# Optimization experiments

Measured on AMD Instinct MI355X. Metric: run time of the kernel, lower is better.

The kernel has to match this reference:

```python
import jax, jax.numpy as jnp
import numpy as np
import math

N = 4096
D = 256


def _xavier(key, shape):
    fan_in, fan_out = shape[0], shape[1]
    std = math.sqrt(2.0 / (fan_in + fan_out))
    return jax.random.normal(key, shape, dtype=jnp.float32) * std


def setup_inputs() -> dict:
    key = jax.random.key(0)
    ks = jax.random.split(key, 12)
    return {
        "cur": jax.random.normal(ks[0], (N, D), dtype=jnp.float32),
        "pre": jax.random.normal(ks[1], (N, D), dtype=jnp.float32),
        # SpatialHyperedge params
        "r_proj_s": _xavier(ks[2], (D, D)),
        "incidence_s": _xavier(ks[3], (N, N - 1)),
        # TemporalHyperedge params
        "r_proj_t": _xavier(ks[4], (D, D)),
        "incidence_t": _xavier(ks[5], (N, N)),
        # HHNodeMP params
        "node_proj": _xavier(ks[6], (D, D)),
        "spa_edge_proj": _xavier(ks[7], (D, D)),
        "tmp_edge_proj": _xavier(ks[8], (D, D)),
        "theta_w": _xavier(ks[9], (D, D)),
        "theta_b": jnp.zeros((D,), dtype=jnp.float32),
    }


def _scatter_slave(vals):
    """Place [N, N-1] per-row slave values into a zero-diagonal [N, N] matrix.
    Row i's k-th slave is column k if k < i else k+1 (all j != i in order)."""
    n = vals.shape[0]
    k = jnp.arange(n - 1)[None, :]
    cols = k + (k >= jnp.arange(n)[:, None])  # [N, N-1] column indices
    rows = jnp.broadcast_to(jnp.arange(n)[:, None], (n, n - 1))
    return jnp.zeros((n, n), dtype=vals.dtype).at[rows.reshape(-1), cols.reshape(-1)].set(vals.reshape(-1))


def _fro(x):
    return jnp.sqrt(jnp.sum(x * x))


def reference(cur, pre, r_proj_s, incidence_s, r_proj_t, incidence_t,
              node_proj, spa_edge_proj, tmp_edge_proj, theta_w, theta_b):
    n, d = cur.shape
    inv_sqrt_d = 1.0 / math.sqrt(d)

    # ---- SpatialHyperedge ----
    Xd = jax.lax.stop_gradient(cur)
    master_s = Xd @ r_proj_s                                   # [N, D]
    M_s_full = _scatter_slave(incidence_s)                     # [N, N], zero diag
    neigh_recon_s = M_s_full @ Xd                              # == bmm over gathered slaves
    spatial_loss = (_fro(master_s - neigh_recon_s) * 0.2
                    + jnp.sum(jnp.abs(incidence_s))
                    + 0.001 * _fro(incidence_s))
    # clamp(min=0) then zero-out entries not strictly > 0  => relu-like
    clipped_s = jnp.where(incidence_s > 0.0, incidence_s, 0.0)
    incidence_all = _scatter_slave(clipped_s) + jnp.eye(n, dtype=cur.dtype)

    # ---- TemporalHyperedge ----
    cur_d = jax.lax.stop_gradient(cur)
    pre_d = jax.lax.stop_gradient(pre)
    master_t = cur_d @ r_proj_t
    neigh_recon_t = incidence_t @ pre_d
    temporal_loss = (_fro(master_t - neigh_recon_t) * 0.2
                     + jnp.sum(jnp.abs(incidence_t))
                     + 0.001 * _fro(incidence_t))
    incidence_t_clipped = jnp.maximum(incidence_t, 0.0)

    # ---- SpatialHyperedgeMP ----
    spa_edge_fea = incidence_all @ cur
    spa_deg = jnp.sum(incidence_all, axis=1, keepdims=True)
    spa_emb = spa_edge_fea / spa_deg                           # [N, D]

    # ---- TemporalHyperedgeMP ----
    tmp_edge_fea = incidence_t_clipped @ pre + cur
    tmp_deg = jnp.sum(incidence_t_clipped, axis=1, keepdims=True) + 1.0
    tmp_emb = tmp_edge_fea / tmp_deg                           # [N, D]

    # ---- HHNodeMP ----
    node_fea = cur @ node_proj
    spa_fea = spa_emb @ spa_edge_proj
    tmp_fea = tmp_emb @ tmp_edge_proj
    spa_attn = jnp.sum(spa_fea * node_fea, axis=1, keepdims=True) * inv_sqrt_d
    tmp_attn = jnp.sum(tmp_fea * node_fea, axis=1, keepdims=True) * inv_sqrt_d
    val = spa_attn * spa_fea + tmp_attn * tmp_fea
    node_emb = jax.nn.relu(val @ theta_w.T + theta_b)          # dropout = identity (eval)

    return node_emb, temporal_loss + spatial_loss
```

## Files before the change

kernel.cpp:

```cpp
#include <hip/hip_runtime.h>
#include <hip/hip_bf16.h>
#include <math.h>

#define NN 4096
#define DD 256

typedef __bf16 bf16x8 __attribute__((ext_vector_type(8)));
typedef short  short8 __attribute__((ext_vector_type(8)));
typedef float  f32x4  __attribute__((ext_vector_type(4)));

#define MFMA16(a, b, c) __builtin_amdgcn_mfma_f32_16x16x32_bf16((a), (b), (c), 0, 0, 0)

__device__ inline bf16x8 brelu(bf16x8 a) {
    short8 s = __builtin_bit_cast(short8, a);
    s = s & ~(s >> 15);
    return __builtin_bit_cast(bf16x8, s);
}

__device__ inline float wave_red(float v) {
#pragma unroll
    for (int o = 32; o > 0; o >>= 1) v += __shfl_down(v, o, 64);
    return v;
}

__device__ inline unsigned short bfbits(float f) {
    return __builtin_bit_cast(unsigned short, (__bf16)f);
}

__global__ __launch_bounds__(256) void k_prep(const float* __restrict__ cur,
                                              const float* __restrict__ pre,
                                              __bf16* __restrict__ cur_bf,
                                              __bf16* __restrict__ curT,
                                              __bf16* __restrict__ preT) {
    const int z = blockIdx.z;
    const int i0 = blockIdx.x * 64, d0 = blockIdx.y * 64;
    const float* src = z ? pre : cur;
    __bf16* dstT = z ? preT : curT;
    __shared__ unsigned short tile[64][72];
    const int t = threadIdx.x;
    const int r = t >> 2, c4 = (t & 3) * 16;
    const float* srow = src + (size_t)(i0 + r) * DD + d0 + c4;
    alignas(16) unsigned short loc[16];
#pragma unroll
    for (int e = 0; e < 4; ++e) {
        float4 v = ((const float4*)srow)[e];
        loc[e * 4 + 0] = bfbits(v.x);
        loc[e * 4 + 1] = bfbits(v.y);
        loc[e * 4 + 2] = bfbits(v.z);
        loc[e * 4 + 3] = bfbits(v.w);
    }
#pragma unroll
    for (int e = 0; e < 16; ++e) tile[r][c4 + e] = loc[e];
    if (z == 0) {
        __bf16* drow = cur_bf + (size_t)(i0 + r) * DD + d0 + c4;
        *(uint4*)drow = *(uint4*)&loc[0];
        *(uint4*)(drow + 8) = *(uint4*)&loc[8];
    }
    __syncthreads();
    alignas(16) unsigned short o[16];
#pragma unroll
    for (int e = 0; e < 16; ++e) o[e] = tile[c4 + e][r];
    __bf16* trow = dstT + (size_t)(d0 + r) * NN + i0 + c4;
    *(uint4*)trow = *(uint4*)&o[0];
    *(uint4*)(trow + 8) = *(uint4*)&o[8];
}

__global__ __launch_bounds__(256) void k_proj(
    const float* __restrict__ a0, const float* __restrict__ a1, const float* __restrict__ a2,
    const float* __restrict__ a3, const float* __restrict__ a4, const float* __restrict__ a5,
    __bf16* __restrict__ o0, __bf16* __restrict__ o1, __bf16* __restrict__ o2,
    __bf16* __restrict__ o3, __bf16* __restrict__ o4, __bf16* __restrict__ o5) {
    const int id = blockIdx.y, r = blockIdx.x, t = threadIdx.x;
    const float* src = id == 0 ? a0 : id == 1 ? a1 : id == 2 ? a2 : id == 3 ? a3 : id == 4 ? a4 : a5;
    __bf16* dst = id == 0 ? o0 : id == 1 ? o1 : id == 2 ? o2 : id == 3 ? o3 : id == 4 ? o4 : o5;
    float v = src[r * DD + t];
    if (id < 5) dst[t * DD + r] = (__bf16)v;
    else        dst[r * DD + t] = (__bf16)v;
}

__global__ __launch_bounds__(256) void k_conv_t(const float* __restrict__ inc,
                                                __bf16* __restrict__ Mbf,
                                                float* __restrict__ rowsum,
                                                float* __restrict__ pAbs, float* __restrict__ pSq) {
    const int i = blockIdx.x, t = threadIdx.x;
    const float4* src = (const float4*)(inc + (size_t)i * NN);
    ushort4* dst = (ushort4*)(Mbf + (size_t)i * NN);
    float rs = 0.f, as = 0.f, qs = 0.f;
#pragma unroll
    for (int e = 0; e < 4; ++e) {
        const int f = t + 256 * e;
        float4 v = src[f];
        float x[4] = {v.x, v.y, v.z, v.w};
        unsigned short o[4];
#pragma unroll
        for (int j = 0; j < 4; ++j) {
            float fv = x[j];
            as += fabsf(fv); qs += fv * fv; rs += fmaxf(fv, 0.f);
            o[j] = bfbits(fv);
        }
        dst[f] = make_ushort4(o[0], o[1], o[2], o[3]);
    }
    __shared__ float red[3][4];
    const int w = t >> 6, lane = t & 63;
    rs = wave_red(rs); as = wave_red(as); qs = wave_red(qs);
    if (lane == 0) { red[0][w] = rs; red[1][w] = as; red[2][w] = qs; }
    __syncthreads();
    if (t == 0) {
        rowsum[i] = red[0][0] + red[0][1] + red[0][2] + red[0][3];
        pAbs[i]   = red[1][0] + red[1][1] + red[1][2] + red[1][3];
        pSq[i]    = red[2][0] + red[2][1] + red[2][2] + red[2][3];
    }
}

__global__ __launch_bounds__(256) void k_conv_s(const float* __restrict__ inc,
                                                __bf16* __restrict__ Mbf,
                                                float* __restrict__ rowsum,
                                                float* __restrict__ pAbs, float* __restrict__ pSq) {
    const int i = blockIdx.x, t = threadIdx.x;
    __shared__ unsigned short row[NN];
    const float* srow = inc + (size_t)i * (NN - 1);
    float rs = 0.f, as = 0.f, qs = 0.f;
#pragma unroll
    for (int e = 0; e < 4; ++e) {
        const int f = t + 256 * e;
        float x[4] = {0.f, 0.f, 0.f, 0.f};
        if (f < 1023) __builtin_memcpy(x, srow + 4 * f, 16);
        else          __builtin_memcpy(x, srow + 4092, 12);
#pragma unroll
        for (int j = 0; j < 4; ++j) {
            const int k = 4 * f + j;
            float fv = x[j];
            as += fabsf(fv); qs += fv * fv; rs += fmaxf(fv, 0.f);
            if (k < NN - 1) row[k + (k >= i)] = bfbits(fv);
        }
    }
    if (t == 0) row[i] = 0;
    __syncthreads();
    uint4* dOut = (uint4*)(Mbf + (size_t)i * NN);
    const uint4* sIn = (const uint4*)row;
    dOut[t] = sIn[t];
    dOut[t + 256] = sIn[t + 256];
    __shared__ float red[3][4];
    const int w = t >> 6, lane = t & 63;
    rs = wave_red(rs); as = wave_red(as); qs = wave_red(qs);
    if (lane == 0) { red[0][w] = rs; red[1][w] = as; red[2][w] = qs; }
    __syncthreads();
    if (t == 0) {
        rowsum[i] = red[0][0] + red[0][1] + red[0][2] + red[0][3];
        pAbs[i]   = red[1][0] + red[1][1] + red[1][2] + red[1][3];
        pSq[i]    = red[2][0] + red[2][1] + red[2][2] + red[2][3];
    }
}

template <int DUAL>
__device__ inline void mfma_step(const __bf16 (&As)[64][72], const __bf16 (&Bs)[64][72],
                                 int wr, int wc, int quad, int l16,
                                 f32x4 (&accR)[2][2], f32x4 (&accL)[2][2]) {
#pragma unroll
    for (int ks = 0; ks < 2; ++ks) {
        const int kc = ks * 32 + quad * 8;
        bf16x8 a0 = *(const bf16x8*)&As[wr * 32 + l16][kc];
        bf16x8 a1 = *(const bf16x8*)&As[wr * 32 + 16 + l16][kc];
        bf16x8 b0 = *(const bf16x8*)&Bs[wc * 32 + l16][kc];
        bf16x8 b1 = *(const bf16x8*)&Bs[wc * 32 + 16 + l16][kc];
        accR[0][0] = MFMA16(a0, b0, accR[0][0]);
        accR[0][1] = MFMA16(a0, b1, accR[0][1]);
        accR[1][0] = MFMA16(a1, b0, accR[1][0]);
        accR[1][1] = MFMA16(a1, b1, accR[1][1]);
        if (DUAL) {
            bf16x8 a0r = brelu(a0), a1r = brelu(a1);
            accL[0][0] = MFMA16(a0r, b0, accL[0][0]);
            accL[0][1] = MFMA16(a0r, b1, accL[0][1]);
            accL[1][0] = MFMA16(a1r, b0, accL[1][0]);
            accL[1][1] = MFMA16(a1r, b1, accL[1][1]);
        }
    }
}

__global__ __launch_bounds__(256) void k_big(const __bf16* __restrict__ Mt, const __bf16* __restrict__ Ms,
                                             const __bf16* __restrict__ preT, const __bf16* __restrict__ curT,
                                             const float* __restrict__ negMt, const float* __restrict__ negMs,
                                             const float* __restrict__ cur,
                                             float* __restrict__ feaT, float* __restrict__ feaS,
                                             float* __restrict__ pDiff) {
    const int z = blockIdx.z;
    const __bf16* A  = z ? Ms : Mt;
    const __bf16* BT = z ? curT : preT;
    const float* negM = z ? negMs : negMt;
    float* fea = z ? feaS : feaT;
    const int n0 = blockIdx.x * 64, m0 = blockIdx.y * 64;
    __shared__ __bf16 As[64][72], Bs[64][72];
    __shared__ float sred[4];
    f32x4 accR[2][2], accL[2][2];
#pragma unroll
    for (int i = 0; i < 2; ++i)
#pragma unroll
        for (int j = 0; j < 2; ++j) { accR[i][j] = (f32x4)0.f; accL[i][j] = (f32x4)0.f; }
    const int t = threadIdx.x, w = t >> 6, lane = t & 63, quad = lane >> 4, l16 = lane & 15;
    const int wr = w >> 1, wc = w & 1;
    const int sr = t >> 2, sc = (t & 3) * 16;
    const __bf16* gA = A + (size_t)(m0 + sr) * NN + sc;
    const __bf16* gB = BT + (size_t)(n0 + sr) * NN + sc;
    for (int kt = 0; kt < NN / 64; ++kt) {
        uint4 av0 = *(const uint4*)(gA);
        uint4 av1 = *(const uint4*)(gA + 8);
        uint4 bv0 = *(const uint4*)(gB);
        uint4 bv1 = *(const uint4*)(gB + 8);
        __syncthreads();
        *(uint4*)&As[sr][sc] = av0; *(uint4*)&As[sr][sc + 8] = av1;
        *(uint4*)&Bs[sr][sc] = bv0; *(uint4*)&Bs[sr][sc + 8] = bv1;
        __syncthreads();
        mfma_step<1>(As, Bs, wr, wc, quad, l16, accR, accL);
        gA += 64; gB += 64;
    }
    float sumd = 0.f;
#pragma unroll
    for (int mi = 0; mi < 2; ++mi)
#pragma unroll
        for (int ni = 0; ni < 2; ++ni)
#pragma unroll
            for (int r = 0; r < 4; ++r) {
                int gr = m0 + wr * 32 + mi * 16 + quad * 4 + r;
                int gc = n0 + wc * 32 + ni * 16 + l16;
                size_t idx = (size_t)gr * DD + gc;
                float diff = accR[mi][ni][r] + negM[idx];
                sumd += diff * diff;
                fea[idx] = accL[mi][ni][r] + cur[idx];
            }
    sumd = wave_red(sumd);
    if (lane == 0) sred[w] = sumd;
    __syncthreads();
    if (t == 0)
        pDiff[z * 256 + blockIdx.y * 4 + blockIdx.x] = sred[0] + sred[1] + sred[2] + sred[3];
}

__global__ __launch_bounds__(256) void k_small3(const __bf16* __restrict__ cur_bf,
                                                const __bf16* __restrict__ pTs, const __bf16* __restrict__ pTt,
                                                const __bf16* __restrict__ pTn,
                                                float* __restrict__ negMs, float* __restrict__ negMt,
                                                float* __restrict__ nodeFea) {
    const int z = blockIdx.z;
    const __bf16* BT = z == 0 ? pTs : (z == 1 ? pTt : pTn);
    const int n0 = blockIdx.x * 64, m0 = blockIdx.y * 64;
    __shared__ __bf16 As[64][72], Bs[64][72];
    f32x4 accR[2][2];
#pragma unroll
    for (int i = 0; i < 2; ++i)
#pragma unroll
        for (int j = 0; j < 2; ++j) accR[i][j] = (f32x4)0.f;
    const int t = threadIdx.x, w = t >> 6, lane = t & 63, quad = lane >> 4, l16 = lane & 15;
    const int wr = w >> 1, wc = w & 1;
    const int sr = t >> 2, sc = (t & 3) * 16;
    const __bf16* gA = cur_bf + (size_t)(m0 + sr) * DD + sc;
    const __bf16* gB = BT + (size_t)(n0 + sr) * DD + sc;
    for (int kt = 0; kt < DD / 64; ++kt) {
        uint4 av0 = *(const uint4*)(gA);
        uint4 av1 = *(const uint4*)(gA + 8);
        uint4 bv0 = *(const uint4*)(gB);
        uint4 bv1 = *(const uint4*)(gB + 8);
        __syncthreads();
        *(uint4*)&As[sr][sc] = av0; *(uint4*)&As[sr][sc + 8] = av1;
        *(uint4*)&Bs[sr][sc] = bv0; *(uint4*)&Bs[sr][sc + 8] = bv1;
        __syncthreads();
        mfma_step<0>(As, Bs, wr, wc, quad, l16, accR, accR);
        gA += 64; gB += 64;
    }
#pragma unroll
    for (int mi = 0; mi < 2; ++mi)
#pragma unroll
        for (int ni = 0; ni < 2; ++ni)
#pragma unroll
            for (int r = 0; r < 4; ++r) {
                int gr = m0 + wr * 32 + mi * 16 + quad * 4 + r;
                int gc = n0 + wc * 32 + ni * 16 + l16;
                size_t idx = (size_t)gr * DD + gc;
                float v = accR[mi][ni][r];
                if (z == 0) negMs[idx] = -v;
                else if (z == 1) negMt[idx] = -v;
                else nodeFea[idx] = v;
            }
}

__global__ __launch_bounds__(256) void k_fea(const float* __restrict__ feaS, const float* __restrict__ feaT,
                                             const float* __restrict__ rsS, const float* __restrict__ rsT,
                                             const __bf16* __restrict__ pTspa, const __bf16* __restrict__ pTtmp,
                                             float* __restrict__ spaF, float* __restrict__ tmpF) {
    const int z = blockIdx.z;
    const float* fea = z ? feaT : feaS;
    const float* rs = z ? rsT : rsS;
    const __bf16* BT = z ? pTtmp : pTspa;
    float* outF = z ? tmpF : spaF;
    const int n0 = blockIdx.x * 64, m0 = blockIdx.y * 64;
    __shared__ __bf16 As[64][72], Bs[64][72];
    f32x4 accR[2][2];
#pragma unroll
    for (int i = 0; i < 2; ++i)
#pragma unroll
        for (int j = 0; j < 2; ++j) accR[i][j] = (f32x4)0.f;
    const int t = threadIdx.x, w = t >> 6, lane = t & 63, quad = lane >> 4, l16 = lane & 15;
    const int wr = w >> 1, wc = w & 1;
    const int sr = t >> 2, sc = (t & 3) * 16;
    const float inv = 1.f / (rs[m0 + sr] + 1.f);
    const float* gA = fea + (size_t)(m0 + sr) * DD + sc;
    const __bf16* gB = BT + (size_t)(n0 + sr) * DD + sc;
    for (int kt = 0; kt < DD / 64; ++kt) {
        __bf16 tmp[16];
#pragma unroll
        for (int e4 = 0; e4 < 4; ++e4) {
            float4 v = ((const float4*)gA)[e4];
            tmp[e4 * 4 + 0] = (__bf16)(v.x * inv);
            tmp[e4 * 4 + 1] = (__bf16)(v.y * inv);
            tmp[e4 * 4 + 2] = (__bf16)(v.z * inv);
            tmp[e4 * 4 + 3] = (__bf16)(v.w * inv);
        }
        uint4 bv0 = *(const uint4*)(gB);
        uint4 bv1 = *(const uint4*)(gB + 8);
        __syncthreads();
        *(uint4*)&As[sr][sc] = *(uint4*)&tmp[0]; *(uint4*)&As[sr][sc + 8] = *(uint4*)&tmp[8];
        *(uint4*)&Bs[sr][sc] = bv0; *(uint4*)&Bs[sr][sc + 8] = bv1;
        __syncthreads();
        mfma_step<0>(As, Bs, wr, wc, quad, l16, accR, accR);
        gA += 64; gB += 64;
    }
#pragma unroll
    for (int mi = 0; mi < 2; ++mi)
#pragma unroll
        for (int ni = 0; ni < 2; ++ni)
#pragma unroll
            for (int r = 0; r < 4; ++r) {
                int gr = m0 + wr * 32 + mi * 16 + quad * 4 + r;
                int gc = n0 + wc * 32 + ni * 16 + l16;
                outF[(size_t)gr * DD + gc] = accR[mi][ni][r];
            }
}

__global__ __launch_bounds__(256) void k_attn(const float* __restrict__ spaF, const float* __restrict__ tmpF,
                                              const float* __restrict__ nodeF,
                                              float* __restrict__ spaA, float* __restrict__ tmpA) {
    const int t = threadIdx.x, w = t >> 6, lane = t & 63;
    const int i = blockIdx.x * 4 + w;
    const float4* sf = (const float4*)(spaF + (size_t)i * DD);
    const float4* tf = (const float4*)(tmpF + (size_t)i * DD);
    const float4* nf = (const float4*)(nodeF + (size_t)i * DD);
    float4 s = sf[lane], p = tf[lane], n = nf[lane];
    float ds = s.x * n.x + s.y * n.y + s.z * n.z + s.w * n.w;
    float dt = p.x * n.x + p.y * n.y + p.z * n.z + p.w * n.w;
    ds = wave_red(ds); dt = wave_red(dt);
    if (lane == 0) { spaA[i] = ds * 0.0625f; tmpA[i] = dt * 0.0625f; }
}

__global__ __launch_bounds__(256) void k_final(const float* __restrict__ spaF, const float* __restrict__ tmpF,
                                               const float* __restrict__ spaA, const float* __restrict__ tmpA,
                                               const __bf16* __restrict__ thetaBf, const float* __restrict__ thetaB,
                                               float* __restrict__ out) {
    const int n0 = blockIdx.x * 64, m0 = blockIdx.y * 64;
    __shared__ __bf16 As[64][72], Bs[64][72];
    f32x4 accR[2][2];
#pragma unroll
    for (int i = 0; i < 2; ++i)
#pragma unroll
        for (int j = 0; j < 2; ++j) accR[i][j] = (f32x4)0.f;
    const int t = threadIdx.x, w = t >> 6, lane = t & 63, quad = lane >> 4, l16 = lane & 15;
    const int wr = w >> 1, wc = w & 1;
    const int sr = t >> 2, sc = (t & 3) * 16;
    const float sa = spaA[m0 + sr], ta = tmpA[m0 + sr];
    const float* gS = spaF + (size_t)(m0 + sr) * DD + sc;
    const float* gT = tmpF + (size_t)(m0 + sr) * DD + sc;
    const __bf16* gB = thetaBf + (size_t)(n0 + sr) * DD + sc;
    for (int kt = 0; kt < DD / 64; ++kt) {
        __bf16 tmp[16];
#pragma unroll
        for (int e4 = 0; e4 < 4; ++e4) {
            float4 vs = ((const float4*)gS)[e4];
            float4 vt = ((const float4*)gT)[e4];
            tmp[e4 * 4 + 0] = (__bf16)(sa * vs.x + ta * vt.x);
            tmp[e4 * 4 + 1] = (__bf16)(sa * vs.y + ta * vt.y);
            tmp[e4 * 4 + 2] = (__bf16)(sa * vs.z + ta * vt.z);
            tmp[e4 * 4 + 3] = (__bf16)(sa * vs.w + ta * vt.w);
        }
        uint4 bv0 = *(const uint4*)(gB);
        uint4 bv1 = *(const uint4*)(gB + 8);
        __syncthreads();
        *(uint4*)&As[sr][sc] = *(uint4*)&tmp[0]; *(uint4*)&As[sr][sc + 8] = *(uint4*)&tmp[8];
        *(uint4*)&Bs[sr][sc] = bv0; *(uint4*)&Bs[sr][sc + 8] = bv1;
        __syncthreads();
        mfma_step<0>(As, Bs, wr, wc, quad, l16, accR, accR);
        gS += 64; gT += 64; gB += 64;
    }
#pragma unroll
    for (int mi = 0; mi < 2; ++mi)
#pragma unroll
        for (int ni = 0; ni < 2; ++ni)
#pragma unroll
            for (int r = 0; r < 4; ++r) {
                int gr = m0 + wr * 32 + mi * 16 + quad * 4 + r;
                int gc = n0 + wc * 32 + ni * 16 + l16;
                float v = accR[mi][ni][r] + thetaB[gc];
                out[(size_t)gr * DD + gc] = fmaxf(v, 0.f);
            }
}

__global__ __launch_bounds__(256) void k_loss(const float* __restrict__ pAbsT, const float* __restrict__ pSqT,
                                              const float* __restrict__ pAbsS, const float* __restrict__ pSqS,
                                              const float* __restrict__ pDiff,
                                              float* __restrict__ out) {
    const int t = threadIdx.x;
    float aT = 0.f, qT = 0.f, aS = 0.f, qS = 0.f;
#pragma unroll
    for (int j = 0; j < 16; ++j) {
        const int i = t + 256 * j;
        aT += pAbsT[i]; qT += pSqT[i]; aS += pAbsS[i]; qS += pSqS[i];
    }
    float dT = pDiff[t], dS = pDiff[256 + t];
    aT = wave_red(aT); qT = wave_red(qT); aS = wave_red(aS); qS = wave_red(qS);
    dT = wave_red(dT); dS = wave_red(dS);
    __shared__ float red[6][4];
    const int w = t >> 6, lane = t & 63;
    if (lane == 0) { red[0][w] = aT; red[1][w] = qT; red[2][w] = aS; red[3][w] = qS; red[4][w] = dT; red[5][w] = dS; }
    __syncthreads();
    if (t == 0) {
        float s[6];
#pragma unroll
        for (int k = 0; k < 6; ++k) s[k] = red[k][0] + red[k][1] + red[k][2] + red[k][3];
        float l = s[0] + 0.001f * sqrtf(s[1]) + 0.2f * sqrtf(s[4])
                + s[2] + 0.001f * sqrtf(s[3]) + 0.2f * sqrtf(s[5]);
        out[(size_t)NN * DD] = l;
    }
}

extern "C" void kernel_launch(void* const* d_in, const int* in_sizes, int n_in,
                              void* d_out, int out_size, void* d_ws, size_t ws_size,
                              hipStream_t stream) {
    (void)in_sizes; (void)n_in; (void)out_size; (void)ws_size;
    const float* cur      = (const float*)d_in[0];
    const float* pre      = (const float*)d_in[1];
    const float* r_proj_s = (const float*)d_in[2];
    const float* inc_s    = (const float*)d_in[3];
    const float* r_proj_t = (const float*)d_in[4];
    const float* inc_t    = (const float*)d_in[5];
    const float* node_pj  = (const float*)d_in[6];
    const float* spa_pj   = (const float*)d_in[7];
    const float* tmp_pj   = (const float*)d_in[8];
    const float* theta_w  = (const float*)d_in[9];
    const float* theta_b  = (const float*)d_in[10];
    float* out = (float*)d_out;

    char* p = (char*)d_ws;
    auto alloc = [&](size_t bytes) -> void* {
        void* r = (void*)p;
        p += (bytes + 255) & ~(size_t)255;
        return r;
    };
    __bf16* Mt      = (__bf16*)alloc((size_t)NN * NN * 2);
    __bf16* Ms      = (__bf16*)alloc((size_t)NN * NN * 2);
    __bf16* cur_bf  = (__bf16*)alloc((size_t)NN * DD * 2);
    __bf16* curT    = (__bf16*)alloc((size_t)NN * DD * 2);
    __bf16* preT    = (__bf16*)alloc((size_t)NN * DD * 2);
    __bf16* pTs     = (__bf16*)alloc((size_t)DD * DD * 2);
    __bf16* pTt     = (__bf16*)alloc((size_t)DD * DD * 2);
    __bf16* pTn     = (__bf16*)alloc((size_t)DD * DD * 2);
    __bf16* pTspa   = (__bf16*)alloc((size_t)DD * DD * 2);
    __bf16* pTtmp   = (__bf16*)alloc((size_t)DD * DD * 2);
    __bf16* thetaBf = (__bf16*)alloc((size_t)DD * DD * 2);
    float* negMs    = (float*)alloc((size_t)NN * DD * 4);
    float* negMt    = (float*)alloc((size_t)NN * DD * 4);
    float* nodeFea  = (float*)alloc((size_t)NN * DD * 4);
    float* feaS     = (float*)alloc((size_t)NN * DD * 4);
    float* feaT     = (float*)alloc((size_t)NN * DD * 4);
    float* spaF     = (float*)alloc((size_t)NN * DD * 4);
    float* tmpF     = (float*)alloc((size_t)NN * DD * 4);
    float* rsS      = (float*)alloc((size_t)NN * 4);
    float* rsT      = (float*)alloc((size_t)NN * 4);
    float* spaA     = (float*)alloc((size_t)NN * 4);
    float* tmpA     = (float*)alloc((size_t)NN * 4);
    float* pAbsT    = (float*)alloc((size_t)NN * 4);
    float* pSqT     = (float*)alloc((size_t)NN * 4);
    float* pAbsS    = (float*)alloc((size_t)NN * 4);
    float* pSqS     = (float*)alloc((size_t)NN * 4);
    float* pDiff    = (float*)alloc(512 * 4);

    k_prep<<<dim3(NN / 64, DD / 64, 2), 256, 0, stream>>>(cur, pre, cur_bf, curT, preT);
    k_proj<<<dim3(DD, 6), 256, 0, stream>>>(r_proj_s, r_proj_t, node_pj, spa_pj, tmp_pj, theta_w,
                                            pTs, pTt, pTn, pTspa, pTtmp, thetaBf);
    k_conv_t<<<NN, 256, 0, stream>>>(inc_t, Mt, rsT, pAbsT, pSqT);
    k_conv_s<<<NN, 256, 0, stream>>>(inc_s, Ms, rsS, pAbsS, pSqS);
    k_small3<<<dim3(4, 64, 3), 256, 0, stream>>>(cur_bf, pTs, pTt, pTn, negMs, negMt, nodeFea);
    k_big<<<dim3(4, 64, 2), 256, 0, stream>>>(Mt, Ms, preT, curT, negMt, negMs, cur, feaT, feaS, pDiff);
    k_fea<<<dim3(4, 64, 2), 256, 0, stream>>>(feaS, feaT, rsS, rsT, pTspa, pTtmp, spaF, tmpF);
    k_attn<<<NN / 4, 256, 0, stream>>>(spaF, tmpF, nodeFea, spaA, tmpA);
    k_final<<<dim3(4, 64), 256, 0, stream>>>(spaF, tmpF, spaA, tmpA, thetaBf, theta_b, out);
    k_loss<<<1, 256, 0, stream>>>(pAbsT, pSqT, pAbsS, pSqS, pDiff, out);
}
```

Measured before the change: 268.8 us.

## Retile big GEMM to full-width 32-row tiles with double-buffered swizzled LDS; merge conv kernels

Measured after the change: 292.5 us. 8.8% more time.

```diff
diff --git a/kernel.cpp b/kernel.cpp
--- a/kernel.cpp
+++ b/kernel.cpp
@@ -78,78 +78,170 @@
     else        dst[r * DD + t] = (__bf16)v;
 }
 
-__global__ __launch_bounds__(256) void k_conv_t(const float* __restrict__ inc,
-                                                __bf16* __restrict__ Mbf,
-                                                float* __restrict__ rowsum,
-                                                float* __restrict__ pAbs, float* __restrict__ pSq) {
-    const int i = blockIdx.x, t = threadIdx.x;
-    const float4* src = (const float4*)(inc + (size_t)i * NN);
-    ushort4* dst = (ushort4*)(Mbf + (size_t)i * NN);
-    float rs = 0.f, as = 0.f, qs = 0.f;
-#pragma unroll
-    for (int e = 0; e < 4; ++e) {
-        const int f = t + 256 * e;
-        float4 v = src[f];
-        float x[4] = {v.x, v.y, v.z, v.w};
-        unsigned short o[4];
-#pragma unroll
-        for (int j = 0; j < 4; ++j) {
-            float fv = x[j];
-            as += fabsf(fv); qs += fv * fv; rs += fmaxf(fv, 0.f);
-            o[j] = bfbits(fv);
-        }
-        dst[f] = make_ushort4(o[0], o[1], o[2], o[3]);
-    }
-    __shared__ float red[3][4];
-    const int w = t >> 6, lane = t & 63;
-    rs = wave_red(rs); as = wave_red(as); qs = wave_red(qs);
-    if (lane == 0) { red[0][w] = rs; red[1][w] = as; red[2][w] = qs; }
-    __syncthreads();
-    if (t == 0) {
-        rowsum[i] = red[0][0] + red[0][1] + red[0][2] + red[0][3];
-        pAbs[i]   = red[1][0] + red[1][1] + red[1][2] + red[1][3];
-        pSq[i]    = red[2][0] + red[2][1] + red[2][2] + red[2][3];
-    }
-}
-
-__global__ __launch_bounds__(256) void k_conv_s(const float* __restrict__ inc,
-                                                __bf16* __restrict__ Mbf,
-                                                float* __restrict__ rowsum,
-                                                float* __restrict__ pAbs, float* __restrict__ pSq) {
+__global__ __launch_bounds__(256) void k_conv(const float* __restrict__ incT, const float* __restrict__ incS,
+                                              __bf16* __restrict__ Mt, __bf16* __restrict__ Ms,
+                                              float* __restrict__ rsT, float* __restrict__ rsS,
+                                              float* __restrict__ pAbsT, float* __restrict__ pSqT,
+                                              float* __restrict__ pAbsS, float* __restrict__ pSqS) {
     const int i = blockIdx.x, t = threadIdx.x;
     __shared__ unsigned short row[NN];
-    const float* srow = inc + (size_t)i * (NN - 1);
+    __shared__ float red[3][4];
     float rs = 0.f, as = 0.f, qs = 0.f;
-#pragma unroll
-    for (int e = 0; e < 4; ++e) {
-        const int f = t + 256 * e;
-        float x[4] = {0.f, 0.f, 0.f, 0.f};
-        if (f < 1023) __builtin_memcpy(x, srow + 4 * f, 16);
-        else          __builtin_memcpy(x, srow + 4092, 12);
-#pragma unroll
-        for (int j = 0; j < 4; ++j) {
-            const int k = 4 * f + j;
-            float fv = x[j];
-            as += fabsf(fv); qs += fv * fv; rs += fmaxf(fv, 0.f);
-            if (k < NN - 1) row[k + (k >= i)] = bfbits(fv);
-        }
-    }
-    if (t == 0) row[i] = 0;
+    if (blockIdx.y == 0) {
+        const float4* src = (const float4*)(incT + (size_t)i * NN);
+        ushort4* dst = (ushort4*)(Mt + (size_t)i * NN);
+#pragma unroll
+        for (int e = 0; e < 4; ++e) {
+            const int f = t + 256 * e;
+            float4 v = src[f];
+            float x[4] = {v.x, v.y, v.z, v.w};
+            unsigned short o[4];
+#pragma unroll
+            for (int j = 0; j < 4; ++j) {
+                float fv = x[j];
+                as += fabsf(fv); qs += fv * fv; rs += fmaxf(fv, 0.f);
+                o[j] = bfbits(fv);
+            }
+            dst[f] = make_ushort4(o[0], o[1], o[2], o[3]);
+        }
+        const int w = t >> 6, lane = t & 63;
+        rs = wave_red(rs); as = wave_red(as); qs = wave_red(qs);
+        if (lane == 0) { red[0][w] = rs; red[1][w] = as; red[2][w] = qs; }
+        __syncthreads();
+        if (t == 0) {
+            rsT[i]   = red[0][0] + red[0][1] + red[0][2] + red[0][3];
+            pAbsT[i] = red[1][0] + red[1][1] + red[1][2] + red[1][3];
+            pSqT[i]  = red[2][0] + red[2][1] + red[2][2] + red[2][3];
+        }
+    } else {
+        const float* srow = incS + (size_t)i * (NN - 1);
+#pragma unroll
+        for (int e = 0; e < 4; ++e) {
+            const int f = t + 256 * e;
+            float x[4] = {0.f, 0.f, 0.f, 0.f};
+            if (f < 1023) __builtin_memcpy(x, srow + 4 * f, 16);
+            else          __builtin_memcpy(x, srow + 4092, 12);
+#pragma unroll
+            for (int j = 0; j < 4; ++j) {
+                const int k = 4 * f + j;
+                float fv = x[j];
+                as += fabsf(fv); qs += fv * fv; rs += fmaxf(fv, 0.f);
+                if (k < NN - 1) row[k + (k >= i)] = bfbits(fv);
+            }
+        }
+        if (t == 0) row[i] = 0;
+        __syncthreads();
+        uint4* dOut = (uint4*)(Ms + (size_t)i * NN);
+        const uint4* sIn = (const uint4*)row;
+        dOut[t] = sIn[t];
+        dOut[t + 256] = sIn[t + 256];
+        const int w = t >> 6, lane = t & 63;
+        rs = wave_red(rs); as = wave_red(as); qs = wave_red(qs);
+        if (lane == 0) { red[0][w] = rs; red[1][w] = as; red[2][w] = qs; }
+        __syncthreads();
+        if (t == 0) {
+            rsS[i]   = red[0][0] + red[0][1] + red[0][2] + red[0][3];
+            pAbsS[i] = red[1][0] + red[1][1] + red[1][2] + red[1][3];
+            pSqS[i]  = red[2][0] + red[2][1] + red[2][2] + red[2][3];
+        }
+    }
+}
+
+__global__ __launch_bounds__(256) void k_big(const __bf16* __restrict__ Mt, const __bf16* __restrict__ Ms,
+                                             const __bf16* __restrict__ preT, const __bf16* __restrict__ curT,
+                                             const float* __restrict__ negMt, const float* __restrict__ negMs,
+                                             const float* __restrict__ cur,
+                                             float* __restrict__ feaT, float* __restrict__ feaS,
+                                             float* __restrict__ pDiff) {
+    const int z = blockIdx.y;
+    const __bf16* A  = z ? Ms : Mt;
+    const __bf16* BT = z ? curT : preT;
+    const float* negM = z ? negMs : negMt;
+    float* fea = z ? feaS : feaT;
+    const int m0 = blockIdx.x * 32;
+    __shared__ __bf16 As[2][32][64];
+    __shared__ float sred[4];
+    const int t = threadIdx.x, w = t >> 6, lane = t & 63, quad = lane >> 4, l16 = lane & 15;
+    const int rsw = l16 & 7;
+    const int srow = t >> 3, sc8 = t & 7;
+    const int swz = (sc8 ^ (srow & 7)) * 8;
+    const __bf16* gA = A + (size_t)(m0 + srow) * NN + sc8 * 8;
+    const int nb = w * 64;
+    const __bf16* gB[4];
+#pragma unroll
+    for (int nf = 0; nf < 4; ++nf)
+        gB[nf] = BT + (size_t)(nb + nf * 16 + l16) * NN + quad * 8;
+
+    f32x4 accR[2][4], accL[2][4];
+#pragma unroll
+    for (int mi = 0; mi < 2; ++mi)
+#pragma unroll
+        for (int nf = 0; nf < 4; ++nf) { accR[mi][nf] = (f32x4)0.f; accL[mi][nf] = (f32x4)0.f; }
+
+    bf16x8 b[2][2][4];
+    uint4 preA;
+    {
+        uint4 a0 = *(const uint4*)gA; gA += 64;
+        *(uint4*)&As[0][srow][swz] = a0;
+        preA = *(const uint4*)gA; gA += 64;
+#pragma unroll
+        for (int ks = 0; ks < 2; ++ks)
+#pragma unroll
+            for (int nf = 0; nf < 4; ++nf)
+                b[0][ks][nf] = *(const bf16x8*)(gB[nf] + ks * 32);
+        __syncthreads();
+    }
+#pragma unroll 2
+    for (int kt = 0; kt < 64; ++kt) {
+        const int cb = kt & 1;
+        if (kt < 63) *(uint4*)&As[cb ^ 1][srow][swz] = preA;
+        if (kt < 62) { preA = *(const uint4*)gA; gA += 64; }
+        if (kt < 63) {
+#pragma unroll
+            for (int ks = 0; ks < 2; ++ks)
+#pragma unroll
+                for (int nf = 0; nf < 4; ++nf)
+                    b[cb ^ 1][ks][nf] = *(const bf16x8*)(gB[nf] + (kt + 1) * 64 + ks * 32);
+        }
+        bf16x8 a[2][2];
+#pragma unroll
+        for (int ks = 0; ks < 2; ++ks) {
+            const int col = ((ks * 4 + quad) ^ rsw) * 8;
+#pragma unroll
+            for (int mi = 0; mi < 2; ++mi)
+                a[ks][mi] = *(const bf16x8*)&As[cb][mi * 16 + l16][col];
+        }
+#pragma unroll
+        for (int ks = 0; ks < 2; ++ks)
+#pragma unroll
+            for (int mi = 0; mi < 2; ++mi) {
+                bf16x8 ar = brelu(a[ks][mi]);
+#pragma unroll
+                for (int nf = 0; nf < 4; ++nf) {
+                    accR[mi][nf] = MFMA16(a[ks][mi], b[cb][ks][nf], accR[mi][nf]);
+                    accL[mi][nf] = MFMA16(ar, b[cb][ks][nf], accL[mi][nf]);
+                }
+            }
+        __syncthreads();
+    }
+    float sumd = 0.f;
+#pragma unroll
+    for (int mi = 0; mi < 2; ++mi)
+#pragma unroll
+        for (int nf = 0; nf < 4; ++nf)
+#pragma unroll
+            for (int r = 0; r < 4; ++r) {
+                int gr = m0 + mi * 16 + quad * 4 + r;
+                int gc = nb + nf * 16 + l16;
+                size_t idx = (size_t)gr * DD + gc;
+                float diff = accR[mi][nf][r] + negM[idx];
+                sumd += diff * diff;
+                fea[idx] = accL[mi][nf][r] + cur[idx];
+            }
+    sumd = wave_red(sumd);
+    if (lane == 0) sred[w] = sumd;
     __syncthreads();
-    uint4* dOut = (uint4*)(Mbf + (size_t)i * NN);
-    const uint4* sIn = (const uint4*)row;
-    dOut[t] = sIn[t];
-    dOut[t + 256] = sIn[t + 256];
-    __shared__ float red[3][4];
-    const int w = t >> 6, lane = t & 63;
-    rs = wave_red(rs); as = wave_red(as); qs = wave_red(qs);
-    if (lane == 0) { red[0][w] = rs; red[1][w] = as; red[2][w] = qs; }
-    __syncthreads();
-    if (t == 0) {
-        rowsum[i] = red[0][0] + red[0][1] + red[0][2] + red[0][3];
-        pAbs[i]   = red[1][0] + red[1][1] + red[1][2] + red[1][3];
-        pSq[i]    = red[2][0] + red[2][1] + red[2][2] + red[2][3];
-    }
+    if (t == 0) pDiff[z * 128 + blockIdx.x] = sred[0] + sred[1] + sred[2] + sred[3];
 }
 
 template <int DUAL>
@@ -177,63 +269,6 @@
     }
 }
 
-__global__ __launch_bounds__(256) void k_big(const __bf16* __restrict__ Mt, const __bf16* __restrict__ Ms,
-                                             const __bf16* __restrict__ preT, const __bf16* __restrict__ curT,
-                                             const float* __restrict__ negMt, const float* __restrict__ negMs,
-                                             const float* __restrict__ cur,
-                                             float* __restrict__ feaT, float* __restrict__ feaS,
-                                             float* __restrict__ pDiff) {
-    const int z = blockIdx.z;
-    const __bf16* A  = z ? Ms : Mt;
-    const __bf16* BT = z ? curT : preT;
-    const float* negM = z ? negMs : negMt;
-    float* fea = z ? feaS : feaT;
-    const int n0 = blockIdx.x * 64, m0 = blockIdx.y * 64;
-    __shared__ __bf16 As[64][72], Bs[64][72];
-    __shared__ float sred[4];
-    f32x4 accR[2][2], accL[2][2];
-#pragma unroll
-    for (int i = 0; i < 2; ++i)
-#pragma unroll
-        for (int j = 0; j < 2; ++j) { accR[i][j] = (f32x4)0.f; accL[i][j] = (f32x4)0.f; }
-    const int t = threadIdx.x, w = t >> 6, lane = t & 63, quad = lane >> 4, l16 = lane & 15;
-    const int wr = w >> 1, wc = w & 1;
-    const int sr = t >> 2, sc = (t & 3) * 16;
-    const __bf16* gA = A + (size_t)(m0 + sr) * NN + sc;
-    const __bf16* gB = BT + (size_t)(n0 + sr) * NN + sc;
-    for (int kt = 0; kt < NN / 64; ++kt) {
-        uint4 av0 = *(const uint4*)(gA);
-        uint4 av1 = *(const uint4*)(gA + 8);
-        uint4 bv0 = *(const uint4*)(gB);
-        uint4 bv1 = *(const uint4*)(gB + 8);
-        __syncthreads();
-        *(uint4*)&As[sr][sc] = av0; *(uint4*)&As[sr][sc + 8] = av1;
-        *(uint4*)&Bs[sr][sc] = bv0; *(uint4*)&Bs[sr][sc + 8] = bv1;
-        __syncthreads();
-        mfma_step<1>(As, Bs, wr, wc, quad, l16, accR, accL);
-        gA += 64; gB += 64;
-    }
-    float sumd = 0.f;
-#pragma unroll
-    for (int mi = 0; mi < 2; ++mi)
-#pragma unroll
-        for (int ni = 0; ni < 2; ++ni)
-#pragma unroll
-            for (int r = 0; r < 4; ++r) {
-                int gr = m0 + wr * 32 + mi * 16 + quad * 4 + r;
-                int gc = n0 + wc * 32 + ni * 16 + l16;
-                size_t idx = (size_t)gr * DD + gc;
-                float diff = accR[mi][ni][r] + negM[idx];
-                sumd += diff * diff;
-                fea[idx] = accL[mi][ni][r] + cur[idx];
-            }
-    sumd = wave_red(sumd);
-    if (lane == 0) sred[w] = sumd;
-    __syncthreads();
-    if (t == 0)
-        pDiff[z * 256 + blockIdx.y * 4 + blockIdx.x] = sred[0] + sred[1] + sred[2] + sred[3];
-}
-
 __global__ __launch_bounds__(256) void k_small3(const __bf16* __restrict__ cur_bf,
                                                 const __bf16* __restrict__ pTs, const __bf16* __restrict__ pTt,
                                                 const __bf16* __restrict__ pTn,
@@ -411,7 +446,9 @@
         const int i = t + 256 * j;
         aT += pAbsT[i]; qT += pSqT[i]; aS += pAbsS[i]; qS += pSqS[i];
     }
-    float dT = pDiff[t], dS = pDiff[256 + t];
+    float pd = pDiff[t];
+    float dT = t < 128 ? pd : 0.f;
+    float dS = t < 128 ? 0.f : pd;
     aT = wave_red(aT); qT = wave_red(qT); aS = wave_red(aS); qS = wave_red(qS);
     dT = wave_red(dT); dS = wave_red(dS);
     __shared__ float red[6][4];
@@ -477,15 +514,14 @@
     float* pSqT     = (float*)alloc((size_t)NN * 4);
     float* pAbsS    = (float*)alloc((size_t)NN * 4);
     float* pSqS     = (float*)alloc((size_t)NN * 4);
-    float* pDiff    = (float*)alloc(512 * 4);
+    float* pDiff    = (float*)alloc(256 * 4);
 
     k_prep<<<dim3(NN / 64, DD / 64, 2), 256, 0, stream>>>(cur, pre, cur_bf, curT, preT);
     k_proj<<<dim3(DD, 6), 256, 0, stream>>>(r_proj_s, r_proj_t, node_pj, spa_pj, tmp_pj, theta_w,
                                             pTs, pTt, pTn, pTspa, pTtmp, thetaBf);
-    k_conv_t<<<NN, 256, 0, stream>>>(inc_t, Mt, rsT, pAbsT, pSqT);
-    k_conv_s<<<NN, 256, 0, stream>>>(inc_s, Ms, rsS, pAbsS, pSqS);
+    k_conv<<<dim3(NN, 2), 256, 0, stream>>>(inc_t, inc_s, Mt, Ms, rsT, rsS, pAbsT, pSqT, pAbsS, pSqS);
     k_small3<<<dim3(4, 64, 3), 256, 0, stream>>>(cur_bf, pTs, pTt, pTn, negMs, negMt, nodeFea);
-    k_big<<<dim3(4, 64, 2), 256, 0, stream>>>(Mt, Ms, preT, curT, negMt, negMs, cur, feaT, feaS, pDiff);
+    k_big<<<dim3(128, 2), 256, 0, stream>>>(Mt, Ms, preT, curT, negMt, negMs, cur, feaT, feaS, pDiff);
     k_fea<<<dim3(4, 64, 2), 256, 0, stream>>>(feaS, feaT, rsS, rsT, pTspa, pTtmp, spaF, tmpF);
     k_attn<<<NN / 4, 256, 0, stream>>>(spaF, tmpF, nodeFea, spaA, tmpA);
     k_final<<<dim3(4, 64), 256, 0, stream>>>(spaF, tmpF, spaA, tmpA, thetaBf, theta_b, out);
```
